# Optimization experiments

Measured on AMD Instinct MI355X. Metric: run time of the kernel, lower is better.

The kernel has to match this reference:

```python
import jax, jax.numpy as jnp
import numpy as np

EPS = 1e-5

def _bn(h, gamma, beta):
    # BatchNorm1d in training mode: biased batch stats over the batch dim
    m = h.mean(axis=0)
    v = h.var(axis=0)
    return gamma * (h - m) * jax.lax.rsqrt(v + EPS) + beta


def setup_inputs() -> dict:
    key = jax.random.key(0)
    ks = jax.random.split(key, 8)
    N, E, D = 100000, 1000000, 64
    x = jax.random.normal(ks[0], (N, D), dtype=jnp.float32)
    pair_features = jax.random.normal(ks[1], (E, D), dtype=jnp.float32)
    pair_index = jax.random.randint(ks[2], (2, E), 0, N, dtype=jnp.int32)
    s = 1.0 / np.sqrt(D)
    W_atom = jax.random.uniform(ks[3], (D, D), jnp.float32, -s, s)
    b_atom = jnp.zeros((D,), jnp.float32)
    g_atom = jnp.ones((D,), jnp.float32)
    be_atom = jnp.zeros((D,), jnp.float32)
    W_pair = jax.random.uniform(ks[4], (D, D), jnp.float32, -s, s)
    b_pair = jnp.zeros((D,), jnp.float32)
    g_pair = jnp.ones((D,), jnp.float32)
    be_pair = jnp.zeros((D,), jnp.float32)
    s2 = 1.0 / np.sqrt(2 * D)
    W_a2p = jax.random.uniform(ks[5], (2 * D, D), jnp.float32, -s2, s2)
    b_a2p = jnp.zeros((D,), jnp.float32)
    return {
        "x": x, "pair_features": pair_features, "pair_index": pair_index,
        "W_atom": W_atom, "b_atom": b_atom, "g_atom": g_atom, "be_atom": be_atom,
        "W_pair": W_pair, "b_pair": b_pair, "g_pair": g_pair, "be_pair": be_pair,
        "W_a2p": W_a2p, "b_a2p": b_a2p,
    }


def reference(x, pair_features, pair_index,
              W_atom, b_atom, g_atom, be_atom,
              W_pair, b_pair, g_pair, be_pair,
              W_a2p, b_a2p):
    # atom path: Linear -> ReLU -> BatchNorm
    atom_out = _bn(jax.nn.relu(x @ W_atom + b_atom), g_atom, be_atom)
    # pair path: gather send/recv atoms, concat, linear
    send = x[pair_index[0]]                       # [E, D]
    recv = x[pair_index[1]]                       # [E, D]
    pair_input = jnp.concatenate([send, recv], axis=-1)  # [E, 2D]
    a2p = pair_input @ W_a2p + b_a2p              # [E, Dp]
    pair_bn = _bn(jax.nn.relu(pair_features @ W_pair + b_pair), g_pair, be_pair)
    return atom_out, a2p + pair_bn
```

## Files before the change

kernel.cpp:

```cpp
#include <hip/hip_runtime.h>

#define D 64
#define EPS 1e-5f

typedef __bf16 bf16x4 __attribute__((ext_vector_type(4)));
typedef __bf16 bf16x8 __attribute__((ext_vector_type(8)));
typedef float  f32x4  __attribute__((ext_vector_type(4)));

#define MFMA(a, b, c) __builtin_amdgcn_mfma_f32_16x16x32_bf16((a), (b), (c), 0, 0, 0)

__global__ void __launch_bounds__(256) stats_gemm_kernel(
    const float* __restrict__ in, const float* __restrict__ W,
    const float* __restrict__ bias, int nrows, float* __restrict__ stats)
{
    __shared__ __bf16 As[128 * 72];
    const int tid = threadIdx.x;
    const int lane = tid & 63, wv = tid >> 6;
    const int q = lane >> 4, l16 = lane & 15;

    bf16x8 Bf[2][4];
#pragma unroll
    for (int ks = 0; ks < 2; ++ks)
#pragma unroll
      for (int nt = 0; nt < 4; ++nt)
#pragma unroll
        for (int j = 0; j < 8; ++j)
          Bf[ks][nt][j] = (__bf16)W[(ks * 32 + q * 8 + j) * 64 + nt * 16 + l16];

    float bc[4];
#pragma unroll
    for (int nt = 0; nt < 4; ++nt) bc[nt] = bias[nt * 16 + l16];

    float s[4] = {0.f, 0.f, 0.f, 0.f}, sq[4] = {0.f, 0.f, 0.f, 0.f};

    const int ntiles = (nrows + 127) >> 7;
    for (int t = blockIdx.x; t < ntiles; t += gridDim.x) {
        const int row0 = t << 7;
#pragma unroll
        for (int i = 0; i < 8; ++i) {
            int f = tid * 4 + i * 1024;
            int r = f >> 6, c = f & 63;
            int row = row0 + r;
            float4 v = (row < nrows) ? *(const float4*)(in + (size_t)row * 64 + c)
                                     : make_float4(0.f, 0.f, 0.f, 0.f);
            bf16x4 h;
            h[0] = (__bf16)v.x; h[1] = (__bf16)v.y;
            h[2] = (__bf16)v.z; h[3] = (__bf16)v.w;
            *(bf16x4*)&As[r * 72 + c] = h;
        }
        __syncthreads();

        f32x4 acc[2][4];
#pragma unroll
        for (int mt = 0; mt < 2; ++mt)
#pragma unroll
          for (int nt = 0; nt < 4; ++nt)
            acc[mt][nt] = (f32x4){0.f, 0.f, 0.f, 0.f};

#pragma unroll
        for (int mt = 0; mt < 2; ++mt) {
            int mrow = wv * 32 + mt * 16 + l16;
            bf16x8 a0 = *(const bf16x8*)&As[mrow * 72 + 0 + q * 8];
            bf16x8 a1 = *(const bf16x8*)&As[mrow * 72 + 32 + q * 8];
#pragma unroll
            for (int nt = 0; nt < 4; ++nt) {
                acc[mt][nt] = MFMA(a0, Bf[0][nt], acc[mt][nt]);
                acc[mt][nt] = MFMA(a1, Bf[1][nt], acc[mt][nt]);
            }
        }
        __syncthreads();

#pragma unroll
        for (int mt = 0; mt < 2; ++mt)
#pragma unroll
          for (int r = 0; r < 4; ++r) {
            int row = row0 + wv * 32 + mt * 16 + q * 4 + r;
            if (row < nrows) {
#pragma unroll
              for (int nt = 0; nt < 4; ++nt) {
                float h = fmaxf(acc[mt][nt][r] + bc[nt], 0.f);
                s[nt] += h;
                sq[nt] = fmaf(h, h, sq[nt]);
              }
            }
          }
    }

#pragma unroll
    for (int nt = 0; nt < 4; ++nt) {
        s[nt]  += __shfl_xor(s[nt], 16, 64);  s[nt]  += __shfl_xor(s[nt], 32, 64);
        sq[nt] += __shfl_xor(sq[nt], 16, 64); sq[nt] += __shfl_xor(sq[nt], 32, 64);
    }
    if (q == 0) {
#pragma unroll
        for (int nt = 0; nt < 4; ++nt) {
            atomicAdd(&stats[nt * 16 + l16], s[nt]);
            atomicAdd(&stats[64 + nt * 16 + l16], sq[nt]);
        }
    }
}

__global__ void finalize_stats_kernel(
    const float* __restrict__ stats,
    const float* __restrict__ g_a, const float* __restrict__ be_a,
    const float* __restrict__ g_p, const float* __restrict__ be_p,
    float n_atom, float n_pair, float* __restrict__ params)
{
    const int t = threadIdx.x;
    const int j = t & 63;
    const bool p = t >= 64;
    const float* st = stats + (p ? 128 : 0);
    const float* g  = p ? g_p  : g_a;
    const float* be = p ? be_p : be_a;
    const float cnt = p ? n_pair : n_atom;
    float m = st[j] / cnt;
    float v = st[64 + j] / cnt - m * m;
    float sc = g[j] * rsqrtf(v + EPS);
    float sh = be[j] - m * sc;
    float* pr = params + (p ? 128 : 0);
    pr[j] = sc;
    pr[64 + j] = sh;
}

__global__ void __launch_bounds__(256) apply_atom_kernel(
    const float* __restrict__ in, const float* __restrict__ W,
    const float* __restrict__ bias, int nrows,
    const float* __restrict__ params, float* __restrict__ out)
{
    __shared__ __bf16 As[128 * 72];
    const int tid = threadIdx.x;
    const int lane = tid & 63, wv = tid >> 6;
    const int q = lane >> 4, l16 = lane & 15;

    bf16x8 Bf[2][4];
#pragma unroll
    for (int ks = 0; ks < 2; ++ks)
#pragma unroll
      for (int nt = 0; nt < 4; ++nt)
#pragma unroll
        for (int j = 0; j < 8; ++j)
          Bf[ks][nt][j] = (__bf16)W[(ks * 32 + q * 8 + j) * 64 + nt * 16 + l16];

    float bc[4], sc[4], sh[4];
#pragma unroll
    for (int nt = 0; nt < 4; ++nt) {
        bc[nt] = bias[nt * 16 + l16];
        sc[nt] = params[nt * 16 + l16];
        sh[nt] = params[64 + nt * 16 + l16];
    }

    const int ntiles = (nrows + 127) >> 7;
    for (int t = blockIdx.x; t < ntiles; t += gridDim.x) {
        const int row0 = t << 7;
#pragma unroll
        for (int i = 0; i < 8; ++i) {
            int f = tid * 4 + i * 1024;
            int r = f >> 6, c = f & 63;
            int row = row0 + r;
            float4 v = (row < nrows) ? *(const float4*)(in + (size_t)row * 64 + c)
                                     : make_float4(0.f, 0.f, 0.f, 0.f);
            bf16x4 h;
            h[0] = (__bf16)v.x; h[1] = (__bf16)v.y;
            h[2] = (__bf16)v.z; h[3] = (__bf16)v.w;
            *(bf16x4*)&As[r * 72 + c] = h;
        }
        __syncthreads();

        f32x4 acc[2][4];
#pragma unroll
        for (int mt = 0; mt < 2; ++mt)
#pragma unroll
          for (int nt = 0; nt < 4; ++nt)
            acc[mt][nt] = (f32x4){0.f, 0.f, 0.f, 0.f};

#pragma unroll
        for (int mt = 0; mt < 2; ++mt) {
            int mrow = wv * 32 + mt * 16 + l16;
            bf16x8 a0 = *(const bf16x8*)&As[mrow * 72 + 0 + q * 8];
            bf16x8 a1 = *(const bf16x8*)&As[mrow * 72 + 32 + q * 8];
#pragma unroll
            for (int nt = 0; nt < 4; ++nt) {
                acc[mt][nt] = MFMA(a0, Bf[0][nt], acc[mt][nt]);
                acc[mt][nt] = MFMA(a1, Bf[1][nt], acc[mt][nt]);
            }
        }
        __syncthreads();

#pragma unroll
        for (int mt = 0; mt < 2; ++mt)
#pragma unroll
          for (int r = 0; r < 4; ++r) {
            int row = row0 + wv * 32 + mt * 16 + q * 4 + r;
            if (row < nrows) {
#pragma unroll
              for (int nt = 0; nt < 4; ++nt) {
                float h = fmaxf(acc[mt][nt][r] + bc[nt], 0.f);
                out[(size_t)row * 64 + nt * 16 + l16] = fmaf(h, sc[nt], sh[nt]);
              }
            }
          }
    }
}

__global__ void __launch_bounds__(256) pair_apply_kernel(
    const float* __restrict__ pf, const float* __restrict__ x,
    const int* __restrict__ pidx,
    const float* __restrict__ Wp, const float* __restrict__ bp,
    const float* __restrict__ Wa, const float* __restrict__ ba,
    int E, const float* __restrict__ params, float* __restrict__ out)
{
    __shared__ __bf16 A1[64 * 72];
    __shared__ __bf16 A2[64 * 136];
    const int tid = threadIdx.x;
    const int lane = tid & 63, wv = tid >> 6;
    const int q = lane >> 4, l16 = lane & 15;

    bf16x8 B1[2][4];
#pragma unroll
    for (int ks = 0; ks < 2; ++ks)
#pragma unroll
      for (int nt = 0; nt < 4; ++nt)
#pragma unroll
        for (int j = 0; j < 8; ++j)
          B1[ks][nt][j] = (__bf16)Wp[(ks * 32 + q * 8 + j) * 64 + nt * 16 + l16];

    bf16x8 B2[4][4];
#pragma unroll
    for (int ks = 0; ks < 4; ++ks)
#pragma unroll
      for (int nt = 0; nt < 4; ++nt)
#pragma unroll
        for (int j = 0; j < 8; ++j)
          B2[ks][nt][j] = (__bf16)Wa[(ks * 32 + q * 8 + j) * 64 + nt * 16 + l16];

    float bpc[4], bac[4], sc[4], sh[4];
#pragma unroll
    for (int nt = 0; nt < 4; ++nt) {
        bpc[nt] = bp[nt * 16 + l16];
        bac[nt] = ba[nt * 16 + l16];
        sc[nt]  = params[nt * 16 + l16];
        sh[nt]  = params[64 + nt * 16 + l16];
    }

    const int ntiles = E >> 6;
    for (int t = blockIdx.x; t < ntiles; t += gridDim.x) {
        const int e0 = t << 6;
#pragma unroll
        for (int i = 0; i < 4; ++i) {
            int f = tid * 4 + i * 1024;
            int r = f >> 6, c = f & 63;
            float4 v = *(const float4*)(pf + (size_t)(e0 + r) * 64 + c);
            bf16x4 h;
            h[0] = (__bf16)v.x; h[1] = (__bf16)v.y;
            h[2] = (__bf16)v.z; h[3] = (__bf16)v.w;
            *(bf16x4*)&A1[r * 72 + c] = h;
        }
        {
            const int sub = tid & 7;
            for (int g = tid >> 3; g < 128; g += 32) {
                int el = g >> 1, half = g & 1;
                int idx = pidx[half * E + e0 + el];
                const float* src = x + (size_t)idx * 64 + sub * 8;
                float4 v0 = *(const float4*)(src);
                float4 v1 = *(const float4*)(src + 4);
                bf16x8 h;
                h[0] = (__bf16)v0.x; h[1] = (__bf16)v0.y;
                h[2] = (__bf16)v0.z; h[3] = (__bf16)v0.w;
                h[4] = (__bf16)v1.x; h[5] = (__bf16)v1.y;
                h[6] = (__bf16)v1.z; h[7] = (__bf16)v1.w;
                *(bf16x8*)&A2[el * 136 + half * 64 + sub * 8] = h;
            }
        }
        __syncthreads();

        f32x4 acc1[4], acc2[4];
#pragma unroll
        for (int nt = 0; nt < 4; ++nt) {
            acc1[nt] = (f32x4){0.f, 0.f, 0.f, 0.f};
            acc2[nt] = (f32x4){0.f, 0.f, 0.f, 0.f};
        }

        const int mrow = wv * 16 + l16;
        {
            bf16x8 a0 = *(const bf16x8*)&A1[mrow * 72 + 0 + q * 8];
            bf16x8 a1 = *(const bf16x8*)&A1[mrow * 72 + 32 + q * 8];
#pragma unroll
            for (int nt = 0; nt < 4; ++nt) {
                acc1[nt] = MFMA(a0, B1[0][nt], acc1[nt]);
                acc1[nt] = MFMA(a1, B1[1][nt], acc1[nt]);
            }
        }
#pragma unroll
        for (int ks = 0; ks < 4; ++ks) {
            bf16x8 a = *(const bf16x8*)&A2[mrow * 136 + ks * 32 + q * 8];
#pragma unroll
            for (int nt = 0; nt < 4; ++nt)
                acc2[nt] = MFMA(a, B2[ks][nt], acc2[nt]);
        }
        __syncthreads();

#pragma unroll
        for (int r = 0; r < 4; ++r) {
            int row = e0 + wv * 16 + q * 4 + r;
#pragma unroll
            for (int nt = 0; nt < 4; ++nt) {
                float h = fmaxf(acc1[nt][r] + bpc[nt], 0.f);
                float val = fmaf(h, sc[nt], sh[nt]) + acc2[nt][r] + bac[nt];
                out[(size_t)row * 64 + nt * 16 + l16] = val;
            }
        }
    }
}

extern "C" void kernel_launch(void* const* d_in, const int* in_sizes, int n_in,
                              void* d_out, int out_size, void* d_ws, size_t ws_size,
                              hipStream_t stream) {
    const float* x       = (const float*)d_in[0];
    const float* pf      = (const float*)d_in[1];
    const int*   pidx    = (const int*)d_in[2];
    const float* W_atom  = (const float*)d_in[3];
    const float* b_atom  = (const float*)d_in[4];
    const float* g_atom  = (const float*)d_in[5];
    const float* be_atom = (const float*)d_in[6];
    const float* W_pair  = (const float*)d_in[7];
    const float* b_pair  = (const float*)d_in[8];
    const float* g_pair  = (const float*)d_in[9];
    const float* be_pair = (const float*)d_in[10];
    const float* W_a2p   = (const float*)d_in[11];
    const float* b_a2p   = (const float*)d_in[12];

    const int N = in_sizes[0] / D;
    const int E = in_sizes[1] / D;

    float* out_atom = (float*)d_out;
    float* out_pair = out_atom + (size_t)N * D;

    float* stats  = (float*)d_ws;
    float* params = stats + 256;

    hipMemsetAsync(d_ws, 0, 256 * sizeof(float), stream);

    int at = (N + 127) / 128, pt = (E + 127) / 128;
    int atg = at < 1024 ? at : 1024;
    int ptg = pt < 2048 ? pt : 2048;

    stats_gemm_kernel<<<atg, 256, 0, stream>>>(x, W_atom, b_atom, N, stats);
    stats_gemm_kernel<<<ptg, 256, 0, stream>>>(pf, W_pair, b_pair, E, stats + 128);
    finalize_stats_kernel<<<1, 128, 0, stream>>>(stats, g_atom, be_atom, g_pair, be_pair,
                                                 (float)N, (float)E, params);
    apply_atom_kernel<<<atg, 256, 0, stream>>>(x, W_atom, b_atom, N, params, out_atom);

    int pag = (E / 64) < 2048 ? (E / 64) : 2048;
    pair_apply_kernel<<<pag, 256, 0, stream>>>(pf, x, pidx, W_pair, b_pair,
                                               W_a2p, b_a2p, E, params + 128, out_pair);
}
```

Baseline: 869.6 us.

## Stash bf16 ReLU activations in output buffer to skip recomputing GEMM in apply pass

The stats pass now writes the post-ReLU activations as bf16 into the output buffer, so the apply passes read those back instead of re-reading the fp32 inputs and redoing the Linear. Both GEMM paths drop shared memory staging and have each wave load its fragments directly from global memory. The pair pass gathers send/recv rows per wave, with nontemporal loads and stores added. The cost is an extra bf16 write and read of the intermediate, and an in-place overlap where each tile reads its bf16 data and then overwrites the same region with fp32 results.

Measured after the change: 824.8 us. 1.05x faster.

```diff
diff --git a/kernel.cpp b/kernel.cpp
--- a/kernel.cpp
+++ b/kernel.cpp
@@ -3,17 +3,19 @@
 #define D 64
 #define EPS 1e-5f
 
-typedef __bf16 bf16x4 __attribute__((ext_vector_type(4)));
 typedef __bf16 bf16x8 __attribute__((ext_vector_type(8)));
 typedef float  f32x4  __attribute__((ext_vector_type(4)));
 
 #define MFMA(a, b, c) __builtin_amdgcn_mfma_f32_16x16x32_bf16((a), (b), (c), 0, 0, 0)
 
-__global__ void __launch_bounds__(256) stats_gemm_kernel(
+static inline int imin(int a, int b) { return a < b ? a : b; }
+
+template <bool NTLOAD>
+__global__ void __launch_bounds__(256) fused_h_stats_kernel(
     const float* __restrict__ in, const float* __restrict__ W,
-    const float* __restrict__ bias, int nrows, float* __restrict__ stats)
-{
-    __shared__ __bf16 As[128 * 72];
+    const float* __restrict__ bias, int nrows,
+    float* __restrict__ stats, __bf16* __restrict__ hout)
+{
     const int tid = threadIdx.x;
     const int lane = tid & 63, wv = tid >> 6;
     const int q = lane >> 4, l16 = lane & 15;
@@ -32,58 +34,65 @@
     for (int nt = 0; nt < 4; ++nt) bc[nt] = bias[nt * 16 + l16];
 
     float s[4] = {0.f, 0.f, 0.f, 0.f}, sq[4] = {0.f, 0.f, 0.f, 0.f};
-
-    const int ntiles = (nrows + 127) >> 7;
-    for (int t = blockIdx.x; t < ntiles; t += gridDim.x) {
-        const int row0 = t << 7;
-#pragma unroll
-        for (int i = 0; i < 8; ++i) {
-            int f = tid * 4 + i * 1024;
-            int r = f >> 6, c = f & 63;
-            int row = row0 + r;
-            float4 v = (row < nrows) ? *(const float4*)(in + (size_t)row * 64 + c)
-                                     : make_float4(0.f, 0.f, 0.f, 0.f);
-            bf16x4 h;
-            h[0] = (__bf16)v.x; h[1] = (__bf16)v.y;
-            h[2] = (__bf16)v.z; h[3] = (__bf16)v.w;
-            *(bf16x4*)&As[r * 72 + c] = h;
-        }
-        __syncthreads();
-
-        f32x4 acc[2][4];
-#pragma unroll
-        for (int mt = 0; mt < 2; ++mt)
-#pragma unroll
-          for (int nt = 0; nt < 4; ++nt)
-            acc[mt][nt] = (f32x4){0.f, 0.f, 0.f, 0.f};
-
+    const f32x4 ZERO = {0.f, 0.f, 0.f, 0.f};
+
+    const int ntiles = (nrows + 31) >> 5;
+    const int stride = gridDim.x << 2;
+    for (int t = (blockIdx.x << 2) + wv; t < ntiles; t += stride) {
+        f32x4 st[2][2][2];
 #pragma unroll
         for (int mt = 0; mt < 2; ++mt) {
-            int mrow = wv * 32 + mt * 16 + l16;
-            bf16x8 a0 = *(const bf16x8*)&As[mrow * 72 + 0 + q * 8];
-            bf16x8 a1 = *(const bf16x8*)&As[mrow * 72 + 32 + q * 8];
-#pragma unroll
-            for (int nt = 0; nt < 4; ++nt) {
-                acc[mt][nt] = MFMA(a0, Bf[0][nt], acc[mt][nt]);
-                acc[mt][nt] = MFMA(a1, Bf[1][nt], acc[mt][nt]);
+            int arow = (t << 5) + mt * 16 + l16;
+            arow = arow < nrows ? arow : nrows - 1;
+            const float* p = in + (size_t)arow * 64 + q * 8;
+#pragma unroll
+            for (int ks = 0; ks < 2; ++ks) {
+                if (NTLOAD) {
+                    st[mt][ks][0] = __builtin_nontemporal_load((const f32x4*)(p + ks * 32));
+                    st[mt][ks][1] = __builtin_nontemporal_load((const f32x4*)(p + ks * 32 + 4));
+                } else {
+                    st[mt][ks][0] = *(const f32x4*)(p + ks * 32);
+                    st[mt][ks][1] = *(const f32x4*)(p + ks * 32 + 4);
+                }
             }
         }
-        __syncthreads();
-
+
+        bf16x8 af[2][2];
 #pragma unroll
         for (int mt = 0; mt < 2; ++mt)
 #pragma unroll
-          for (int r = 0; r < 4; ++r) {
-            int row = row0 + wv * 32 + mt * 16 + q * 4 + r;
-            if (row < nrows) {
-#pragma unroll
-              for (int nt = 0; nt < 4; ++nt) {
+          for (int ks = 0; ks < 2; ++ks)
+#pragma unroll
+            for (int j = 0; j < 8; ++j)
+              af[mt][ks][j] = (__bf16)st[mt][ks][j >> 2][j & 3];
+
+        f32x4 acc[2][4];
+#pragma unroll
+        for (int mt = 0; mt < 2; ++mt)
+#pragma unroll
+          for (int nt = 0; nt < 4; ++nt) {
+            acc[mt][nt] = MFMA(af[mt][0], Bf[0][nt], ZERO);
+            acc[mt][nt] = MFMA(af[mt][1], Bf[1][nt], acc[mt][nt]);
+          }
+
+#pragma unroll
+        for (int mt = 0; mt < 2; ++mt) {
+            bf16x8 hh[2];
+#pragma unroll
+            for (int nt = 0; nt < 4; ++nt)
+#pragma unroll
+              for (int r = 0; r < 4; ++r) {
+                const int row = (t << 5) + mt * 16 + q * 4 + r;
                 float h = fmaxf(acc[mt][nt][r] + bc[nt], 0.f);
-                s[nt] += h;
-                sq[nt] = fmaf(h, h, sq[nt]);
+                if (row < nrows) { s[nt] += h; sq[nt] = fmaf(h, h, sq[nt]); }
+                hh[nt >> 1][(nt & 1) * 4 + r] = (__bf16)h;
               }
+            if (((2 * t + mt) << 4) < nrows) {
+                __bf16* dst = hout + ((size_t)(2 * t + mt) * 2048 + lane * 16);
+                *(bf16x8*)dst = hh[0];
+                *(bf16x8*)(dst + 8) = hh[1];
             }
-          }
+        }
     }
 
 #pragma unroll
@@ -123,107 +132,49 @@
 }
 
 __global__ void __launch_bounds__(256) apply_atom_kernel(
-    const float* __restrict__ in, const float* __restrict__ W,
-    const float* __restrict__ bias, int nrows,
-    const float* __restrict__ params, float* __restrict__ out)
-{
-    __shared__ __bf16 As[128 * 72];
+    float* __restrict__ out, const float* __restrict__ params, int nrows)
+{
     const int tid = threadIdx.x;
     const int lane = tid & 63, wv = tid >> 6;
     const int q = lane >> 4, l16 = lane & 15;
 
-    bf16x8 Bf[2][4];
-#pragma unroll
-    for (int ks = 0; ks < 2; ++ks)
-#pragma unroll
-      for (int nt = 0; nt < 4; ++nt)
-#pragma unroll
-        for (int j = 0; j < 8; ++j)
-          Bf[ks][nt][j] = (__bf16)W[(ks * 32 + q * 8 + j) * 64 + nt * 16 + l16];
-
-    float bc[4], sc[4], sh[4];
+    float sc[4], sh[4];
 #pragma unroll
     for (int nt = 0; nt < 4; ++nt) {
-        bc[nt] = bias[nt * 16 + l16];
         sc[nt] = params[nt * 16 + l16];
         sh[nt] = params[64 + nt * 16 + l16];
     }
 
-    const int ntiles = (nrows + 127) >> 7;
-    for (int t = blockIdx.x; t < ntiles; t += gridDim.x) {
-        const int row0 = t << 7;
-#pragma unroll
-        for (int i = 0; i < 8; ++i) {
-            int f = tid * 4 + i * 1024;
-            int r = f >> 6, c = f & 63;
-            int row = row0 + r;
-            float4 v = (row < nrows) ? *(const float4*)(in + (size_t)row * 64 + c)
-                                     : make_float4(0.f, 0.f, 0.f, 0.f);
-            bf16x4 h;
-            h[0] = (__bf16)v.x; h[1] = (__bf16)v.y;
-            h[2] = (__bf16)v.z; h[3] = (__bf16)v.w;
-            *(bf16x4*)&As[r * 72 + c] = h;
-        }
-        __syncthreads();
-
-        f32x4 acc[2][4];
-#pragma unroll
-        for (int mt = 0; mt < 2; ++mt)
-#pragma unroll
-          for (int nt = 0; nt < 4; ++nt)
-            acc[mt][nt] = (f32x4){0.f, 0.f, 0.f, 0.f};
-
-#pragma unroll
-        for (int mt = 0; mt < 2; ++mt) {
-            int mrow = wv * 32 + mt * 16 + l16;
-            bf16x8 a0 = *(const bf16x8*)&As[mrow * 72 + 0 + q * 8];
-            bf16x8 a1 = *(const bf16x8*)&As[mrow * 72 + 32 + q * 8];
-#pragma unroll
-            for (int nt = 0; nt < 4; ++nt) {
-                acc[mt][nt] = MFMA(a0, Bf[0][nt], acc[mt][nt]);
-                acc[mt][nt] = MFMA(a1, Bf[1][nt], acc[mt][nt]);
-            }
-        }
-        __syncthreads();
-
-#pragma unroll
-        for (int mt = 0; mt < 2; ++mt)
+    const int ntiles = (nrows + 15) >> 4;
+    const int stride = gridDim.x << 2;
+    for (int t = (blockIdx.x << 2) + wv; t < ntiles; t += stride) {
+        const __bf16* src = (const __bf16*)out + ((size_t)t * 2048 + lane * 16);
+        bf16x8 h0 = *(const bf16x8*)src;
+        bf16x8 h1 = *(const bf16x8*)(src + 8);
+        asm volatile("s_waitcnt vmcnt(0)" ::: "memory");
+#pragma unroll
+        for (int nt = 0; nt < 4; ++nt)
 #pragma unroll
           for (int r = 0; r < 4; ++r) {
-            int row = row0 + wv * 32 + mt * 16 + q * 4 + r;
-            if (row < nrows) {
-#pragma unroll
-              for (int nt = 0; nt < 4; ++nt) {
-                float h = fmaxf(acc[mt][nt][r] + bc[nt], 0.f);
-                out[(size_t)row * 64 + nt * 16 + l16] = fmaf(h, sc[nt], sh[nt]);
-              }
-            }
+            const int row = (t << 4) + q * 4 + r;
+            float h = (float)((nt < 2) ? h0[nt * 4 + r] : h1[(nt - 2) * 4 + r]);
+            if (row < nrows)
+                __builtin_nontemporal_store(fmaf(h, sc[nt], sh[nt]),
+                                            out + (size_t)row * 64 + nt * 16 + l16);
           }
     }
 }
 
-__global__ void __launch_bounds__(256) pair_apply_kernel(
-    const float* __restrict__ pf, const float* __restrict__ x,
+__global__ void __launch_bounds__(256) pair_pass2_kernel(
+    float* __restrict__ out, const float* __restrict__ x,
     const int* __restrict__ pidx,
-    const float* __restrict__ Wp, const float* __restrict__ bp,
     const float* __restrict__ Wa, const float* __restrict__ ba,
-    int E, const float* __restrict__ params, float* __restrict__ out)
-{
-    __shared__ __bf16 A1[64 * 72];
-    __shared__ __bf16 A2[64 * 136];
+    int E, const float* __restrict__ params)
+{
     const int tid = threadIdx.x;
     const int lane = tid & 63, wv = tid >> 6;
     const int q = lane >> 4, l16 = lane & 15;
 
-    bf16x8 B1[2][4];
-#pragma unroll
-    for (int ks = 0; ks < 2; ++ks)
-#pragma unroll
-      for (int nt = 0; nt < 4; ++nt)
-#pragma unroll
-        for (int j = 0; j < 8; ++j)
-          B1[ks][nt][j] = (__bf16)Wp[(ks * 32 + q * 8 + j) * 64 + nt * 16 + l16];
-
     bf16x8 B2[4][4];
 #pragma unroll
     for (int ks = 0; ks < 4; ++ks)
@@ -233,82 +184,61 @@
         for (int j = 0; j < 8; ++j)
           B2[ks][nt][j] = (__bf16)Wa[(ks * 32 + q * 8 + j) * 64 + nt * 16 + l16];
 
-    float bpc[4], bac[4], sc[4], sh[4];
+    float bac[4], sc[4], sh[4];
 #pragma unroll
     for (int nt = 0; nt < 4; ++nt) {
-        bpc[nt] = bp[nt * 16 + l16];
         bac[nt] = ba[nt * 16 + l16];
         sc[nt]  = params[nt * 16 + l16];
         sh[nt]  = params[64 + nt * 16 + l16];
     }
 
-    const int ntiles = E >> 6;
-    for (int t = blockIdx.x; t < ntiles; t += gridDim.x) {
-        const int e0 = t << 6;
-#pragma unroll
-        for (int i = 0; i < 4; ++i) {
-            int f = tid * 4 + i * 1024;
-            int r = f >> 6, c = f & 63;
-            float4 v = *(const float4*)(pf + (size_t)(e0 + r) * 64 + c);
-            bf16x4 h;
-            h[0] = (__bf16)v.x; h[1] = (__bf16)v.y;
-            h[2] = (__bf16)v.z; h[3] = (__bf16)v.w;
-            *(bf16x4*)&A1[r * 72 + c] = h;
-        }
-        {
-            const int sub = tid & 7;
-            for (int g = tid >> 3; g < 128; g += 32) {
-                int el = g >> 1, half = g & 1;
-                int idx = pidx[half * E + e0 + el];
-                const float* src = x + (size_t)idx * 64 + sub * 8;
-                float4 v0 = *(const float4*)(src);
-                float4 v1 = *(const float4*)(src + 4);
-                bf16x8 h;
-                h[0] = (__bf16)v0.x; h[1] = (__bf16)v0.y;
-                h[2] = (__bf16)v0.z; h[3] = (__bf16)v0.w;
-                h[4] = (__bf16)v1.x; h[5] = (__bf16)v1.y;
-                h[6] = (__bf16)v1.z; h[7] = (__bf16)v1.w;
-                *(bf16x8*)&A2[el * 136 + half * 64 + sub * 8] = h;
-            }
-        }
-        __syncthreads();
-
-        f32x4 acc1[4], acc2[4];
-#pragma unroll
-        for (int nt = 0; nt < 4; ++nt) {
-            acc1[nt] = (f32x4){0.f, 0.f, 0.f, 0.f};
-            acc2[nt] = (f32x4){0.f, 0.f, 0.f, 0.f};
-        }
-
-        const int mrow = wv * 16 + l16;
-        {
-            bf16x8 a0 = *(const bf16x8*)&A1[mrow * 72 + 0 + q * 8];
-            bf16x8 a1 = *(const bf16x8*)&A1[mrow * 72 + 32 + q * 8];
-#pragma unroll
-            for (int nt = 0; nt < 4; ++nt) {
-                acc1[nt] = MFMA(a0, B1[0][nt], acc1[nt]);
-                acc1[nt] = MFMA(a1, B1[1][nt], acc1[nt]);
-            }
-        }
-#pragma unroll
-        for (int ks = 0; ks < 4; ++ks) {
-            bf16x8 a = *(const bf16x8*)&A2[mrow * 136 + ks * 32 + q * 8];
-#pragma unroll
-            for (int nt = 0; nt < 4; ++nt)
-                acc2[nt] = MFMA(a, B2[ks][nt], acc2[nt]);
-        }
-        __syncthreads();
-
-#pragma unroll
-        for (int r = 0; r < 4; ++r) {
-            int row = e0 + wv * 16 + q * 4 + r;
-#pragma unroll
-            for (int nt = 0; nt < 4; ++nt) {
-                float h = fmaxf(acc1[nt][r] + bpc[nt], 0.f);
-                float val = fmaf(h, sc[nt], sh[nt]) + acc2[nt][r] + bac[nt];
-                out[(size_t)row * 64 + nt * 16 + l16] = val;
-            }
-        }
+    const f32x4 ZERO = {0.f, 0.f, 0.f, 0.f};
+
+    const int ntiles = E >> 4;
+    const int stride = gridDim.x << 2;
+    for (int t = (blockIdx.x << 2) + wv; t < ntiles; t += stride) {
+        const int e0 = t << 4;
+        const int se = pidx[e0 + l16];
+        const int re = pidx[E + e0 + l16];
+        const float* ps = x + (size_t)se * 64 + q * 8;
+        const float* pr = x + (size_t)re * 64 + q * 8;
+
+        f32x4 g[4][2];
+        g[0][0] = *(const f32x4*)ps;          g[0][1] = *(const f32x4*)(ps + 4);
+        g[1][0] = *(const f32x4*)(ps + 32);   g[1][1] = *(const f32x4*)(ps + 36);
+        g[2][0] = *(const f32x4*)pr;          g[2][1] = *(const f32x4*)(pr + 4);
+        g[3][0] = *(const f32x4*)(pr + 32);   g[3][1] = *(const f32x4*)(pr + 36);
+
+        const __bf16* hsrc = (const __bf16*)out + ((size_t)t * 2048 + lane * 16);
+        bf16x8 h0 = *(const bf16x8*)hsrc;
+        bf16x8 h1 = *(const bf16x8*)(hsrc + 8);
+
+        bf16x8 af[4];
+#pragma unroll
+        for (int ks = 0; ks < 4; ++ks)
+#pragma unroll
+          for (int j = 0; j < 8; ++j)
+            af[ks][j] = (__bf16)g[ks][j >> 2][j & 3];
+
+        f32x4 acc[4];
+#pragma unroll
+        for (int nt = 0; nt < 4; ++nt) acc[nt] = ZERO;
+#pragma unroll
+        for (int ks = 0; ks < 4; ++ks)
+#pragma unroll
+          for (int nt = 0; nt < 4; ++nt)
+            acc[nt] = MFMA(af[ks], B2[ks][nt], acc[nt]);
+
+        asm volatile("s_waitcnt vmcnt(0)" ::: "memory");
+#pragma unroll
+        for (int nt = 0; nt < 4; ++nt)
+#pragma unroll
+          for (int r = 0; r < 4; ++r) {
+            float h = (float)((nt < 2) ? h0[nt * 4 + r] : h1[(nt - 2) * 4 + r]);
+            float val = fmaf(h, sc[nt], sh[nt]) + acc[nt][r] + bac[nt];
+            __builtin_nontemporal_store(val,
+                out + (size_t)(e0 + q * 4 + r) * 64 + nt * 16 + l16);
+          }
     }
 }
 
@@ -338,19 +268,24 @@
     float* stats  = (float*)d_ws;
     float* params = stats + 256;
 
-    hipMemsetAsync(d_ws, 0, 256 * sizeof(float), stream);
-
-    int at = (N + 127) / 128, pt = (E + 127) / 128;
-    int atg = at < 1024 ? at : 1024;
-    int ptg = pt < 2048 ? pt : 2048;
-
-    stats_gemm_kernel<<<atg, 256, 0, stream>>>(x, W_atom, b_atom, N, stats);
-    stats_gemm_kernel<<<ptg, 256, 0, stream>>>(pf, W_pair, b_pair, E, stats + 128);
-    finalize_stats_kernel<<<1, 128, 0, stream>>>(stats, g_atom, be_atom, g_pair, be_pair,
+    (void)hipMemsetAsync(d_ws, 0, 256 * sizeof(float), stream);
+
+    const int ta = (N + 31) / 32, tp = (E + 31) / 32;
+    const int ga = imin((ta + 3) / 4, 2048);
+    const int gp = imin((tp + 3) / 4, 2048);
+
+    fused_h_stats_kernel<false><<<ga, 256, 0, stream>>>(
+        x, W_atom, b_atom, N, stats, (__bf16*)out_atom);
+    fused_h_stats_kernel<true><<<gp, 256, 0, stream>>>(
+        pf, W_pair, b_pair, E, stats + 128, (__bf16*)out_pair);
+
+    finalize_stats_kernel<<<1, 128, 0, stream>>>(stats, g_atom, be_atom,
+                                                 g_pair, be_pair,
                                                  (float)N, (float)E, params);
-    apply_atom_kernel<<<atg, 256, 0, stream>>>(x, W_atom, b_atom, N, params, out_atom);
-
-    int pag = (E / 64) < 2048 ? (E / 64) : 2048;
-    pair_apply_kernel<<<pag, 256, 0, stream>>>(pf, x, pidx, W_pair, b_pair,
-                                               W_a2p, b_a2p, E, params + 128, out_pair);
-}
+
+    const int t16a = (N + 15) / 16, t16p = E / 16;
+    apply_atom_kernel<<<imin((t16a + 3) / 4, 2048), 256, 0, stream>>>(
+        out_atom, params, N);
+    pair_pass2_kernel<<<imin((t16p + 3) / 4, 2048), 256, 0, stream>>>(
+        out_pair, x, pidx, W_a2p, b_a2p, E, params + 128);
+}
```
